# Kernel optimization log

Hardware: AMD Instinct MI355X
Metric: run time of the kernel (lower is better)

## Reference

```python
import jax, jax.numpy as jnp
import numpy as np

LAYERS = 30
LAYERS_PER_STACK = 10  # layers // stacks
UP_SCALES = (10, 8)


def setup_inputs() -> dict:
    key = jax.random.key(0)
    ks = jax.random.split(key, 12)
    B, T_c, C_in = 4, 400, 80
    T = T_c * UP_SCALES[0] * UP_SCALES[1]  # 32000
    OUT_CH, RES_CH, GATE_CH, SKIP_CH = 256, 64, 128, 64
    s = 0.05  # small init scale to keep gates unsaturated
    inp = {
        "x": jax.random.randint(ks[0], (B, T), 0, OUT_CH, dtype=jnp.int64),
        "c": jax.random.normal(ks[1], (B, C_in, T_c), dtype=jnp.float32),
        "first_w": jax.random.normal(ks[2], (RES_CH, OUT_CH), dtype=jnp.float32) * s,
        "first_b": jnp.zeros((RES_CH,), dtype=jnp.float32),
        "dconv_w": jax.random.normal(ks[3], (LAYERS, GATE_CH, RES_CH, 2), dtype=jnp.float32) * s,
        "dconv_b": jnp.zeros((LAYERS, GATE_CH), dtype=jnp.float32),
        "cond_w": jax.random.normal(ks[4], (LAYERS, GATE_CH, C_in), dtype=jnp.float32) * s,
        "skip_w": jax.random.normal(ks[5], (LAYERS, SKIP_CH, GATE_CH // 2), dtype=jnp.float32) * s,
        "skip_b": jnp.zeros((LAYERS, SKIP_CH), dtype=jnp.float32),
        "out_w": jax.random.normal(ks[6], (LAYERS, RES_CH, GATE_CH // 2), dtype=jnp.float32) * s,
        "out_b": jnp.zeros((LAYERS, RES_CH), dtype=jnp.float32),
        "last_w1": jax.random.normal(ks[7], (SKIP_CH, SKIP_CH), dtype=jnp.float32) * s,
        "last_b1": jnp.zeros((SKIP_CH,), dtype=jnp.float32),
        "last_w2": jax.random.normal(ks[8], (OUT_CH, SKIP_CH), dtype=jnp.float32) * s,
        "last_b2": jnp.zeros((OUT_CH,), dtype=jnp.float32),
        "conv_in_w": jax.random.normal(ks[9], (C_in, C_in), dtype=jnp.float32) * s,
        "up_w0": jnp.full((2 * UP_SCALES[0] + 1,), 1.0 / (2 * UP_SCALES[0] + 1), dtype=jnp.float32),
        "up_w1": jnp.full((2 * UP_SCALES[1] + 1,), 1.0 / (2 * UP_SCALES[1] + 1), dtype=jnp.float32),
    }
    return inp


def _upsample(c, conv_in_w, up_ws):
    # conv_in: 1x1 (aux_context_window=0)
    c = jnp.einsum('oc,bct->bot', conv_in_w, c)
    for w, scale in zip(up_ws, UP_SCALES):
        c = jnp.repeat(c, scale, axis=-1)  # nearest-neighbor upsample along time
        B, C, T = c.shape
        k = w.shape[0]
        c = jax.lax.conv_general_dilated(
            c.reshape(B * C, 1, T), w.reshape(1, 1, k),
            window_strides=(1,), padding=[(scale, scale)],
        ).reshape(B, C, T)
    return c


def reference(x, c, first_w, first_b, dconv_w, dconv_b, cond_w, skip_w, skip_b,
              out_w, out_b, last_w1, last_b1, last_w2, last_b2, conv_in_w, up_w0, up_w1):
    B, T = x.shape
    c_up = _upsample(c, conv_in_w, (up_w0, up_w1))  # (B, 80, T)
    # first_conv on one-hot(x): gather columns of first_w -> (B, 64, T)
    h = first_w.T[x].transpose(0, 2, 1) + first_b[None, :, None]
    skips = jnp.zeros_like(h[:, :1, :1])  # broadcastable accumulator
    skips = 0.0
    for l in range(LAYERS):
        d = 2 ** (l % LAYERS_PER_STACK)
        # causal dilated conv, kernel_size=2: y[t] = W0 @ h[t-d] + W1 @ h[t]
        h_prev = jnp.pad(h, ((0, 0), (0, 0), (d, 0)))[:, :, :T]
        y = (jnp.einsum('oc,bct->bot', dconv_w[l, :, :, 0], h_prev)
             + jnp.einsum('oc,bct->bot', dconv_w[l, :, :, 1], h)
             + dconv_b[l][None, :, None]
             + jnp.einsum('oc,bct->bot', cond_w[l], c_up))
        a, g = jnp.split(y, 2, axis=1)
        z = jnp.tanh(a) * jax.nn.sigmoid(g)  # gated activation, (B, 64, T)
        skips = skips + jnp.einsum('oc,bct->bot', skip_w[l], z) + skip_b[l][None, :, None]
        h = jnp.einsum('oc,bct->bot', out_w[l], z) + out_b[l][None, :, None] + h
    out = jax.nn.relu(skips)
    out = jnp.einsum('oc,bct->bot', last_w1, out) + last_b1[None, :, None]
    out = jax.nn.relu(out)
    out = jnp.einsum('oc,bct->bot', last_w2, out) + last_b2[None, :, None]
    return out  # (B, 256, T) logits
```

## Files before the change

### kernel.cpp

```cpp
#include <hip/hip_runtime.h>

#define TF 32000

typedef short s8v __attribute__((ext_vector_type(8)));
typedef float f4v __attribute__((ext_vector_type(4)));

__device__ __forceinline__ float us2f(unsigned int u16) {
  union { float f; unsigned int i; } v; v.i = u16 << 16; return v.f;
}
__device__ __forceinline__ unsigned short f2b(float f) {
  union { float f; unsigned int u; } v; v.f = f;
  unsigned int u = v.u;
  u = (u + 0x7fffu + ((u >> 16) & 1u)) >> 16;
  return (unsigned short)u;
}

__global__ void k_probe_x(const int* __restrict__ x, int* __restrict__ flag) {
  int acc = 0;
  for (int i = blockIdx.x * 256 + threadIdx.x; i < 64000; i += 32 * 256)
    acc |= x[2 * i + 1];
  unsigned long long m = __ballot(acc != 0);
  if ((threadIdx.x & 63) == 0 && m != 0ULL) atomicOr(flag, 1);
}

__global__ void k_probe_dt(const unsigned short* __restrict__ fw, int* __restrict__ flag) {
  int i = blockIdx.x * 256 + threadIdx.x;
  float v = us2f(fw[i]);
  int bad = !(fabsf(v) <= 1.0f);
  unsigned long long m = __ballot(bad);
  if ((threadIdx.x & 63) == 0 && m != 0ULL) atomicOr(flag, 2);
}

struct SrcPtrs { const void* p[17]; };

__global__ __launch_bounds__(256) void k_cvt(SrcPtrs sp, const int* __restrict__ flag,
                                             float* __restrict__ wdst, float* __restrict__ cdst) {
  int i = blockIdx.x * 256 + threadIdx.x;
  if (i >= 1223846) return;
  const bool f32 = ((*flag) & 2) != 0;
  int s, base;
  if (i < 507968) {
    if (i < 16384)       { s = 0;  base = 0; }
    else if (i < 16448)  { s = 1;  base = 16384; }
    else                 { s = 2;  base = 16448; }
  } else if (i < 943808) {
    if (i < 511808)      { s = 3;  base = 507968; }
    else if (i < 819008) { s = 4;  base = 511808; }
    else if (i < 941888) { s = 5;  base = 819008; }
    else                 { s = 6;  base = 941888; }
  } else if (i < 1089408) {
    if (i < 1066688)      { s = 7;  base = 943808; }
    else if (i < 1068608) { s = 8;  base = 1066688; }
    else if (i < 1072704) { s = 9;  base = 1068608; }
    else if (i < 1072768) { s = 10; base = 1072704; }
    else if (i < 1089152) { s = 11; base = 1072768; }
    else                  { s = 12; base = 1089152; }
  } else {
    if (i < 1095808)      { s = 13; base = 1089408; }
    else if (i < 1095829) { s = 14; base = 1095808; }
    else if (i < 1095846) { s = 15; base = 1095829; }
    else                  { s = 16; base = 1095846; }
  }
  int j = i - base;
  const void* src = sp.p[s];
  float v = f32 ? ((const float*)src)[j] : us2f(((const unsigned short*)src)[j]);
  if (s == 16) cdst[j] = v; else wdst[i] = v;
}

__global__ __launch_bounds__(256) void k_pack(const float* __restrict__ wc,
    unsigned short* __restrict__ w1h, unsigned short* __restrict__ w1l,
    unsigned short* __restrict__ w2h, unsigned short* __restrict__ w2l) {
  int i = blockIdx.x * 256 + threadIdx.x;
  if (i < 860160) {
    int l = i / 28672, r = i % 28672, o = r / 224, k = r % 224;
    float v = 0.f;
    if (k < 128)      v = wc[16448 + l * 16384 + o * 128 + (k & 63) * 2 + (k >> 6)];
    else if (k < 208) v = wc[511808 + l * 10240 + o * 80 + (k - 128)];
    unsigned short hh = f2b(v);
    w1h[i] = hh;
    w1l[i] = f2b(v - us2f(hh));
  } else if (i < 1105920) {
    int j = i - 860160;
    int l = j / 8192, r = j % 8192, o = r / 64, ch = r % 64;
    float v = (o < 64) ? wc[819008 + l * 4096 + o * 64 + ch]
                       : wc[943808 + l * 4096 + (o - 64) * 64 + ch];
    unsigned short hh = f2b(v);
    w2h[j] = hh;
    w2l[j] = f2b(v - us2f(hh));
  }
}

__global__ void k_convin(const float* __restrict__ c, const float* __restrict__ w,
                         float* __restrict__ c0) {
  int b = blockIdx.x / 400, t = blockIdx.x % 400;
  int o = threadIdx.x;
  if (o >= 80) return;
  const float* crow = c + b * 80 * 400 + t;
  const float* wrow = w + o * 80;
  float acc = 0.f;
  for (int k = 0; k < 80; ++k) acc += wrow[k] * crow[k * 400];
  c0[(b * 80 + o) * 400 + t] = acc;
}

__global__ void k_up1(const float* __restrict__ c0, const float* __restrict__ w,
                      float* __restrict__ s1) {
  int id = blockIdx.x * 256 + threadIdx.x;
  int t = id % 4000;
  int bc = id / 4000;
  const float* src = c0 + bc * 400;
  float acc = 0.f;
  #pragma unroll
  for (int j = 0; j < 21; ++j) {
    int tt = t - 10 + j;
    if (tt >= 0 && tt < 4000) acc += w[j] * src[tt / 10];
  }
  s1[id] = acc;
}

__global__ void k_up2(const float* __restrict__ s1, const float* __restrict__ w,
                      unsigned short* __restrict__ cup) {
  int id = blockIdx.x * 256 + threadIdx.x;
  int t = id % TF;
  int bc = id / TF;
  const float* src = s1 + bc * 4000;
  float acc = 0.f;
  #pragma unroll
  for (int j = 0; j < 17; ++j) {
    int tt = t - 8 + j;
    if (tt >= 0 && tt < TF) acc += w[j] * src[tt / 8];
  }
  cup[id] = f2b(acc);
}

__global__ void k_first(const int* __restrict__ x, const int* __restrict__ flag,
                        const float* __restrict__ fw, const float* __restrict__ fb,
                        float* __restrict__ h) {
  int id = blockIdx.x * 256 + threadIdx.x;
  int t = id % TF;
  int r = (id / TF) & 63;
  int b = id / (64 * TF);
  int i = b * TF + t;
  int idx = (((*flag) & 1) ? x[i] : x[2 * i]) & 255;
  h[id] = fw[r * 256 + idx] + fb[r];
}

__global__ __launch_bounds__(256, 3) void k_layer(
    const float* __restrict__ h_in, float* __restrict__ h_out,
    float* __restrict__ skips, const unsigned short* __restrict__ cup,
    const unsigned short* __restrict__ w1h, const unsigned short* __restrict__ w1l,
    const unsigned short* __restrict__ w2h, const unsigned short* __restrict__ w2l,
    const float* __restrict__ db, const float* __restrict__ sb,
    const float* __restrict__ ob, int d, int mode) {
  __shared__ __align__(16) unsigned char smem[47104];
  unsigned short (*Xhi)[232] = (unsigned short (*)[232])smem;
  unsigned short (*Xlo)[136] = (unsigned short (*)[136])(smem + 29696);
  unsigned short (*Zhi)[72]  = (unsigned short (*)[72])smem;
  unsigned short (*Zlo)[72]  = (unsigned short (*)[72])(smem + 9216);
  const int b = blockIdx.x / 500;
  const int t0 = (blockIdx.x % 500) * 64;
  const int tid = threadIdx.x;
  const float* hb = h_in + (size_t)b * 64 * TF;

  const bool d4 = (d & 3) == 0;
  for (int u = tid; u < 1024; u += 256) {
    const int arr = u >> 9, rem = u & 511, cp = rem >> 4, tq = rem & 15;
    const int ch0 = cp * 2;
    float va[4], vb[4];
    if (arr == 0) {
      float4 A = *(const float4*)(hb + ch0 * TF + t0 + tq * 4);
      float4 B = *(const float4*)(hb + (ch0 + 1) * TF + t0 + tq * 4);
      va[0] = A.x; va[1] = A.y; va[2] = A.z; va[3] = A.w;
      vb[0] = B.x; vb[1] = B.y; vb[2] = B.z; vb[3] = B.w;
    } else {
      const int base = t0 - d + tq * 4;
      if (d4 && base >= 0) {
        float4 A = *(const float4*)(hb + ch0 * TF + base);
        float4 B = *(const float4*)(hb + (ch0 + 1) * TF + base);
        va[0] = A.x; va[1] = A.y; va[2] = A.z; va[3] = A.w;
        vb[0] = B.x; vb[1] = B.y; vb[2] = B.z; vb[3] = B.w;
      } else {
        #pragma unroll
        for (int j = 0; j < 4; ++j) {
          int tp = base + j;
          va[j] = tp >= 0 ? hb[ch0 * TF + tp] : 0.f;
          vb[j] = tp >= 0 ? hb[(ch0 + 1) * TF + tp] : 0.f;
        }
      }
    }
    const int colb = (arr == 0 ? 64 : 0) + ch0;
    #pragma unroll
    for (int j = 0; j < 4; ++j) {
      int t = tq * 4 + j;
      unsigned int h0 = f2b(va[j]), h1 = f2b(vb[j]);
      float l0 = va[j] - us2f(h0), l1 = vb[j] - us2f(h1);
      *(unsigned int*)&Xhi[t][colb] = h0 | (h1 << 16);
      *(unsigned int*)&Xlo[t][colb] = (unsigned int)f2b(l0) | ((unsigned int)f2b(l1) << 16);
    }
  }
  const unsigned short* cb = cup + (size_t)b * 80 * TF;
  for (int u = tid; u < 640; u += 256) {
    const int cp = u >> 4, tq = u & 15, cc0 = cp * 2;
    const unsigned int* pa = (const unsigned int*)(cb + cc0 * TF + t0 + tq * 4);
    const unsigned int* pb = (const unsigned int*)(cb + (cc0 + 1) * TF + t0 + tq * 4);
    unsigned int a0 = pa[0], a1 = pa[1], b0 = pb[0], b1 = pb[1];
    const int colb = 128 + cc0, tb = tq * 4;
    *(unsigned int*)&Xhi[tb + 0][colb] = (a0 & 0xffffu) | (b0 << 16);
    *(unsigned int*)&Xhi[tb + 1][colb] = (a0 >> 16) | (b0 & 0xffff0000u);
    *(unsigned int*)&Xhi[tb + 2][colb] = (a1 & 0xffffu) | (b1 << 16);
    *(unsigned int*)&Xhi[tb + 3][colb] = (a1 >> 16) | (b1 & 0xffff0000u);
  }
  if (tid < 64) {
    s8v z = {0, 0, 0, 0, 0, 0, 0, 0};
    *(s8v*)&Xhi[tid][208] = z;
    *(s8v*)&Xhi[tid][216] = z;
  }
  __syncthreads();

  const int wv = tid >> 6, l15 = tid & 15, kl = (tid >> 4) & 3;
  const int R0 = wv * 16, R1 = 64 + wv * 16;
  const int ko = kl * 8;

  f4v accA[4], accG[4];
  {
    f4v bA = *(const f4v*)(db + R0 + kl * 4);
    f4v bG = *(const f4v*)(db + R1 + kl * 4);
    #pragma unroll
    for (int ct = 0; ct < 4; ++ct) { accA[ct] = bA; accG[ct] = bG; }
  }
  #pragma unroll
  for (int s = 0; s < 4; ++s) {
    const int k0 = s * 32 + ko;
    s8v ah0 = *(const s8v*)(w1h + (R0 + l15) * 224 + k0);
    s8v ah1 = *(const s8v*)(w1h + (R1 + l15) * 224 + k0);
    s8v al0 = *(const s8v*)(w1l + (R0 + l15) * 224 + k0);
    s8v al1 = *(const s8v*)(w1l + (R1 + l15) * 224 + k0);
    #pragma unroll
    for (int ct = 0; ct < 4; ++ct) {
      s8v bh = *(const s8v*)&Xhi[ct * 16 + l15][k0];
      s8v bl = *(const s8v*)&Xlo[ct * 16 + l15][k0];
      accA[ct] = __builtin_amdgcn_mfma_f32_16x16x32_bf16(ah0, bh, accA[ct], 0, 0, 0);
      accG[ct] = __builtin_amdgcn_mfma_f32_16x16x32_bf16(ah1, bh, accG[ct], 0, 0, 0);
      accA[ct] = __builtin_amdgcn_mfma_f32_16x16x32_bf16(al0, bh, accA[ct], 0, 0, 0);
      accG[ct] = __builtin_amdgcn_mfma_f32_16x16x32_bf16(al1, bh, accG[ct], 0, 0, 0);
      accA[ct] = __builtin_amdgcn_mfma_f32_16x16x32_bf16(ah0, bl, accA[ct], 0, 0, 0);
      accG[ct] = __builtin_amdgcn_mfma_f32_16x16x32_bf16(ah1, bl, accG[ct], 0, 0, 0);
    }
  }
  #pragma unroll
  for (int s = 4; s < 7; ++s) {
    const int k0 = s * 32 + ko;
    s8v ah0 = *(const s8v*)(w1h + (R0 + l15) * 224 + k0);
    s8v ah1 = *(const s8v*)(w1h + (R1 + l15) * 224 + k0);
    s8v al0 = *(const s8v*)(w1l + (R0 + l15) * 224 + k0);
    s8v al1 = *(const s8v*)(w1l + (R1 + l15) * 224 + k0);
    #pragma unroll
    for (int ct = 0; ct < 4; ++ct) {
      s8v bh = *(const s8v*)&Xhi[ct * 16 + l15][k0];
      accA[ct] = __builtin_amdgcn_mfma_f32_16x16x32_bf16(ah0, bh, accA[ct], 0, 0, 0);
      accG[ct] = __builtin_amdgcn_mfma_f32_16x16x32_bf16(ah1, bh, accG[ct], 0, 0, 0);
      accA[ct] = __builtin_amdgcn_mfma_f32_16x16x32_bf16(al0, bh, accA[ct], 0, 0, 0);
      accG[ct] = __builtin_amdgcn_mfma_f32_16x16x32_bf16(al1, bh, accG[ct], 0, 0, 0);
    }
  }

  float rres[16];
  #pragma unroll
  for (int ct = 0; ct < 4; ++ct) {
    const int t = ct * 16 + l15;
    uint2 rh = *(const uint2*)&Xhi[t][64 + R0 + kl * 4];
    uint2 rl = *(const uint2*)&Xlo[t][64 + R0 + kl * 4];
    rres[ct * 4 + 0] = us2f(rh.x & 0xffffu) + us2f(rl.x & 0xffffu);
    rres[ct * 4 + 1] = us2f(rh.x >> 16)     + us2f(rl.x >> 16);
    rres[ct * 4 + 2] = us2f(rh.y & 0xffffu) + us2f(rl.y & 0xffffu);
    rres[ct * 4 + 3] = us2f(rh.y >> 16)     + us2f(rl.y >> 16);
  }
  __syncthreads();

  #pragma unroll
  for (int ct = 0; ct < 4; ++ct) {
    const int t = ct * 16 + l15;
    unsigned int hw[2], lw[2];
    #pragma unroll
    for (int p = 0; p < 2; ++p) {
      float a0 = accA[ct][2 * p],     g0 = accG[ct][2 * p];
      float a1 = accA[ct][2 * p + 1], g1 = accG[ct][2 * p + 1];
      float z0 = tanhf(a0) / (1.f + expf(-g0));
      float z1 = tanhf(a1) / (1.f + expf(-g1));
      unsigned int h0 = f2b(z0), h1 = f2b(z1);
      hw[p] = h0 | (h1 << 16);
      lw[p] = (unsigned int)f2b(z0 - us2f(h0)) | ((unsigned int)f2b(z1 - us2f(h1)) << 16);
    }
    uint2 hv; hv.x = hw[0]; hv.y = hw[1];
    uint2 lv; lv.x = lw[0]; lv.y = lw[1];
    *(uint2*)&Zhi[t][R0 + kl * 4] = hv;
    *(uint2*)&Zlo[t][R0 + kl * 4] = lv;
  }
  __syncthreads();

  f4v accS[4], accH[4];
  {
    f4v bS = *(const f4v*)(sb + R0 + kl * 4);
    f4v bO = *(const f4v*)(ob + R0 + kl * 4);
    #pragma unroll
    for (int ct = 0; ct < 4; ++ct) { accS[ct] = bS; accH[ct] = bO; }
  }
  #pragma unroll
  for (int s = 0; s < 2; ++s) {
    const int k0 = s * 32 + ko;
    s8v ah0 = *(const s8v*)(w2h + (R0 + l15) * 64 + k0);
    s8v ah1 = *(const s8v*)(w2h + (R1 + l15) * 64 + k0);
    s8v al0 = *(const s8v*)(w2l + (R0 + l15) * 64 + k0);
    s8v al1 = *(const s8v*)(w2l + (R1 + l15) * 64 + k0);
    #pragma unroll
    for (int ct = 0; ct < 4; ++ct) {
      s8v bh = *(const s8v*)&Zhi[ct * 16 + l15][k0];
      s8v bl = *(const s8v*)&Zlo[ct * 16 + l15][k0];
      accS[ct] = __builtin_amdgcn_mfma_f32_16x16x32_bf16(ah0, bh, accS[ct], 0, 0, 0);
      accH[ct] = __builtin_amdgcn_mfma_f32_16x16x32_bf16(ah1, bh, accH[ct], 0, 0, 0);
      accS[ct] = __builtin_amdgcn_mfma_f32_16x16x32_bf16(al0, bh, accS[ct], 0, 0, 0);
      accH[ct] = __builtin_amdgcn_mfma_f32_16x16x32_bf16(al1, bh, accH[ct], 0, 0, 0);
      accS[ct] = __builtin_amdgcn_mfma_f32_16x16x32_bf16(ah0, bl, accS[ct], 0, 0, 0);
      accH[ct] = __builtin_amdgcn_mfma_f32_16x16x32_bf16(ah1, bl, accH[ct], 0, 0, 0);
    }
  }

  float* sp_ = skips + ((size_t)b * 64 + R0 + kl * 4) * TF + t0;
  float* hp_ = h_out + ((size_t)b * 64 + R0 + kl * 4) * TF + t0;
  #pragma unroll
  for (int ct = 0; ct < 4; ++ct) {
    const int t = ct * 16 + l15;
    if (mode & 1) {
      sp_[0 * TF + t] = accS[ct][0];
      sp_[1 * TF + t] = accS[ct][1];
      sp_[2 * TF + t] = accS[ct][2];
      sp_[3 * TF + t] = accS[ct][3];
    } else {
      sp_[0 * TF + t] += accS[ct][0];
      sp_[1 * TF + t] += accS[ct][1];
      sp_[2 * TF + t] += accS[ct][2];
      sp_[3 * TF + t] += accS[ct][3];
    }
    if (!(mode & 2)) {
      hp_[0 * TF + t] = accH[ct][0] + rres[ct * 4 + 0];
      hp_[1 * TF + t] = accH[ct][1] + rres[ct * 4 + 1];
      hp_[2 * TF + t] = accH[ct][2] + rres[ct * 4 + 2];
      hp_[3 * TF + t] = accH[ct][3] + rres[ct * 4 + 3];
    }
  }
}

__global__ __launch_bounds__(256, 4) void k_final(
    const float* __restrict__ skips,
    const float* __restrict__ w1, const float* __restrict__ b1,
    const float* __restrict__ w2, const float* __restrict__ b2,
    float* __restrict__ out) {
  __shared__ __align__(16) unsigned short Shi[64][72];
  __shared__ __align__(16) unsigned short Slo[64][72];
  __shared__ __align__(16) unsigned short Zhi[64][72];
  __shared__ __align__(16) unsigned short Zlo[64][72];
  const int b = blockIdx.x / 500;
  const int t0 = (blockIdx.x % 500) * 64;
  const int tid = threadIdx.x;
  const float* sbase = skips + (size_t)b * 64 * TF;

  for (int u = tid; u < 512; u += 256) {
    const int cp = u >> 4, tq = u & 15, ch0 = cp * 2;
    float4 A = *(const float4*)(sbase + (size_t)ch0 * TF + t0 + tq * 4);
    float4 B = *(const float4*)(sbase + (size_t)(ch0 + 1) * TF + t0 + tq * 4);
    float va[4] = {fmaxf(A.x, 0.f), fmaxf(A.y, 0.f), fmaxf(A.z, 0.f), fmaxf(A.w, 0.f)};
    float vb[4] = {fmaxf(B.x, 0.f), fmaxf(B.y, 0.f), fmaxf(B.z, 0.f), fmaxf(B.w, 0.f)};
    #pragma unroll
    for (int j = 0; j < 4; ++j) {
      int t = tq * 4 + j;
      unsigned int h0 = f2b(va[j]), h1 = f2b(vb[j]);
      *(unsigned int*)&Shi[t][ch0] = h0 | (h1 << 16);
      *(unsigned int*)&Slo[t][ch0] =
          (unsigned int)f2b(va[j] - us2f(h0)) | ((unsigned int)f2b(vb[j] - us2f(h1)) << 16);
    }
  }
  __syncthreads();

  const int wv = tid >> 6, l15 = tid & 15, kl = (tid >> 4) & 3;
  const int R = wv * 16;

  f4v acc[4];
  {
    f4v bb = *(const f4v*)(b1 + R + kl * 4);
    #pragma unroll
    for (int ct = 0; ct < 4; ++ct) acc[ct] = bb;
  }
  #pragma unroll
  for (int ks = 0; ks < 2; ++ks) {
    const int k0 = ks * 32 + kl * 8;
    const float* wr = w1 + (R + l15) * 64 + k0;
    s8v ah, al;
    #pragma unroll
    for (int m = 0; m < 8; ++m) {
      float v = wr[m];
      unsigned short hh = f2b(v);
      ah[m] = (short)hh;
      al[m] = (short)f2b(v - us2f(hh));
    }
    #pragma unroll
    for (int ct = 0; ct < 4; ++ct) {
      s8v bh = *(const s8v*)&Shi[ct * 16 + l15][k0];
      s8v bl = *(const s8v*)&Slo[ct * 16 + l15][k0];
      acc[ct] = __builtin_amdgcn_mfma_f32_16x16x32_bf16(ah, bh, acc[ct], 0, 0, 0);
      acc[ct] = __builtin_amdgcn_mfma_f32_16x16x32_bf16(al, bh, acc[ct], 0, 0, 0);
      acc[ct] = __builtin_amdgcn_mfma_f32_16x16x32_bf16(ah, bl, acc[ct], 0, 0, 0);
    }
  }
  #pragma unroll
  for (int ct = 0; ct < 4; ++ct) {
    const int t = ct * 16 + l15;
    unsigned int hw[2], lw[2];
    #pragma unroll
    for (int p = 0; p < 2; ++p) {
      float z0 = fmaxf(acc[ct][2 * p], 0.f);
      float z1 = fmaxf(acc[ct][2 * p + 1], 0.f);
      unsigned int h0 = f2b(z0), h1 = f2b(z1);
      hw[p] = h0 | (h1 << 16);
      lw[p] = (unsigned int)f2b(z0 - us2f(h0)) | ((unsigned int)f2b(z1 - us2f(h1)) << 16);
    }
    uint2 hv; hv.x = hw[0]; hv.y = hw[1];
    uint2 lv; lv.x = lw[0]; lv.y = lw[1];
    *(uint2*)&Zhi[t][R + kl * 4] = hv;
    *(uint2*)&Zlo[t][R + kl * 4] = lv;
  }
  __syncthreads();

  float* obase = out + (size_t)b * 256 * TF + t0;
  #pragma unroll
  for (int g = 0; g < 4; ++g) {
    const int R2 = g * 64 + wv * 16;
    f4v a2[4];
    {
      f4v bb = *(const f4v*)(b2 + R2 + kl * 4);
      #pragma unroll
      for (int ct = 0; ct < 4; ++ct) a2[ct] = bb;
    }
    #pragma unroll
    for (int ks = 0; ks < 2; ++ks) {
      const int k0 = ks * 32 + kl * 8;
      const float* wr = w2 + (R2 + l15) * 64 + k0;
      s8v ah, al;
      #pragma unroll
      for (int m = 0; m < 8; ++m) {
        float v = wr[m];
        unsigned short hh = f2b(v);
        ah[m] = (short)hh;
        al[m] = (short)f2b(v - us2f(hh));
      }
      #pragma unroll
      for (int ct = 0; ct < 4; ++ct) {
        s8v bh = *(const s8v*)&Zhi[ct * 16 + l15][k0];
        s8v bl = *(const s8v*)&Zlo[ct * 16 + l15][k0];
        a2[ct] = __builtin_amdgcn_mfma_f32_16x16x32_bf16(ah, bh, a2[ct], 0, 0, 0);
        a2[ct] = __builtin_amdgcn_mfma_f32_16x16x32_bf16(al, bh, a2[ct], 0, 0, 0);
        a2[ct] = __builtin_amdgcn_mfma_f32_16x16x32_bf16(ah, bl, a2[ct], 0, 0, 0);
      }
    }
    const int r0 = R2 + kl * 4;
    #pragma unroll
    for (int ct = 0; ct < 4; ++ct) {
      const int t = ct * 16 + l15;
      obase[(size_t)(r0 + 0) * TF + t] = a2[ct][0];
      obase[(size_t)(r0 + 1) * TF + t] = a2[ct][1];
      obase[(size_t)(r0 + 2) * TF + t] = a2[ct][2];
      obase[(size_t)(r0 + 3) * TF + t] = a2[ct][3];
    }
  }
}

extern "C" void kernel_launch(void* const* d_in, const int* in_sizes, int n_in,
                              void* d_out, int out_size, void* d_ws, size_t ws_size,
                              hipStream_t stream) {
  const int* x = (const int*)d_in[0];

  float* ws = (float*)d_ws;
  int*   flag = (int*)ws;
  float* wcan = ws + 16;
  unsigned short* cupb = (unsigned short*)(ws + 1095872);
  float* ha    = ws + 6215872;
  float* hbuf  = ws + 14407872;
  float* skips = ws + 22599872;
  float* cin = ha;
  float* c0  = ha + 128000;
  float* s1f = ha + 256000;
  if (ws_size < (size_t)30791872 * 4) return;

  float* fwc = wcan;            float* fbc = wcan + 16384;
  float* dbc = wcan + 507968;
  float* sbc = wcan + 941888;
  float* obc = wcan + 1066688;  float* w1c = wcan + 1068608;
  float* b1c = wcan + 1072704;  float* w2c = wcan + 1072768;
  float* b2c = wcan + 1089152;  float* ciwc = wcan + 1089408;
  float* uw0c = wcan + 1095808; float* uw1c = wcan + 1095829;

  unsigned short* wp = (unsigned short*)d_out;
  unsigned short* W1H = wp;
  unsigned short* W1L = wp + 860160;
  unsigned short* W2H = wp + 1720320;
  unsigned short* W2L = wp + 1966080;

  hipMemsetAsync(flag, 0, 64, stream);
  k_probe_x<<<dim3(32), dim3(256), 0, stream>>>(x, flag);
  k_probe_dt<<<dim3(64), dim3(256), 0, stream>>>((const unsigned short*)d_in[2], flag);

  SrcPtrs sp;
  sp.p[0] = d_in[2];  sp.p[1] = d_in[3];  sp.p[2] = d_in[4];  sp.p[3] = d_in[5];
  sp.p[4] = d_in[6];  sp.p[5] = d_in[7];  sp.p[6] = d_in[8];  sp.p[7] = d_in[9];
  sp.p[8] = d_in[10]; sp.p[9] = d_in[11]; sp.p[10] = d_in[12]; sp.p[11] = d_in[13];
  sp.p[12] = d_in[14]; sp.p[13] = d_in[15]; sp.p[14] = d_in[16]; sp.p[15] = d_in[17];
  sp.p[16] = d_in[1];
  k_cvt<<<dim3(4781), dim3(256), 0, stream>>>(sp, flag, wcan, cin);
  k_pack<<<dim3(4320), dim3(256), 0, stream>>>(wcan, W1H, W1L, W2H, W2L);

  k_convin<<<dim3(1600), dim3(128), 0, stream>>>(cin, ciwc, c0);
  k_up1<<<dim3(5000), dim3(256), 0, stream>>>(c0, uw0c, s1f);
  k_up2<<<dim3(40000), dim3(256), 0, stream>>>(s1f, uw1c, cupb);
  k_first<<<dim3(32000), dim3(256), 0, stream>>>(x, flag, fwc, fbc, ha);

  float* hin = ha; float* hout = hbuf;
  for (int l = 0; l < 30; ++l) {
    int d = 1 << (l % 10);
    int mode = (l == 0 ? 1 : 0) | (l == 29 ? 2 : 0);
    k_layer<<<dim3(2000), dim3(256), 0, stream>>>(
        hin, hout, skips, cupb,
        W1H + (size_t)l * 28672, W1L + (size_t)l * 28672,
        W2H + (size_t)l * 8192,  W2L + (size_t)l * 8192,
        dbc + l * 128, sbc + l * 64, obc + l * 64, d, mode);
    float* t = hin; hin = hout; hout = t;
  }
  k_final<<<dim3(2000), dim3(256), 0, stream>>>(skips, w1c, b1c, w2c, b2c,
                                                (float*)d_out);
}
```

Measured before the change: 1.938 ms.

## Store residual state as pre-split channel-paired bf16 hi/lo and use fast gate math

The residual stream h is now kept between layers as channel-pair-packed bf16 hi/lo words instead of fp32. Each layer loads those words with 16-byte vector loads straight into shared memory, and the hi/lo split moves to the producer's epilogue. The conditioning tensor is packed by channel pairs in the same way. Load index mapping is reorganised for coalescing, and tanh*sigmoid is replaced with a clamped exp/rcp formulation. The goal is less per-layer conversion ALU work and simpler loads, at the cost of slightly different gate accuracy.

```diff
diff --git a/kernel.cpp b/kernel.cpp
--- a/kernel.cpp
+++ b/kernel.cpp
@@ -4,6 +4,7 @@
 
 typedef short s8v __attribute__((ext_vector_type(8)));
 typedef float f4v __attribute__((ext_vector_type(4)));
+typedef unsigned int ui4 __attribute__((ext_vector_type(4)));
 
 __device__ __forceinline__ float us2f(unsigned int u16) {
   union { float f; unsigned int i; } v; v.i = u16 << 16; return v.f;
@@ -13,6 +14,12 @@
   unsigned int u = v.u;
   u = (u + 0x7fffu + ((u >> 16) & 1u)) >> 16;
   return (unsigned short)u;
+}
+__device__ __forceinline__ float gatef(float a, float g) {
+  a = fminf(fmaxf(a, -15.f), 15.f);
+  float ta = __expf(2.f * a);
+  float sg = __expf(-g);
+  return (ta - 1.f) * __builtin_amdgcn_rcpf((ta + 1.f) * (1.f + sg));
 }
 
 __global__ void k_probe_x(const int* __restrict__ x, int* __restrict__ flag) {
@@ -118,35 +125,47 @@
 }
 
 __global__ void k_up2(const float* __restrict__ s1, const float* __restrict__ w,
-                      unsigned short* __restrict__ cup) {
+                      unsigned int* __restrict__ cpk) {
   int id = blockIdx.x * 256 + threadIdx.x;
   int t = id % TF;
-  int bc = id / TF;
-  const float* src = s1 + bc * 4000;
-  float acc = 0.f;
+  int cp = (id / TF) % 40;
+  int b = id / (40 * TF);
+  const float* src0 = s1 + (b * 80 + cp * 2) * 4000;
+  const float* src1 = src0 + 4000;
+  float a0 = 0.f, a1 = 0.f;
   #pragma unroll
   for (int j = 0; j < 17; ++j) {
     int tt = t - 8 + j;
-    if (tt >= 0 && tt < TF) acc += w[j] * src[tt / 8];
-  }
-  cup[id] = f2b(acc);
+    if (tt >= 0 && tt < TF) {
+      int q = tt / 8;
+      a0 += w[j] * src0[q];
+      a1 += w[j] * src1[q];
+    }
+  }
+  cpk[id] = (unsigned int)f2b(a0) | ((unsigned int)f2b(a1) << 16);
 }
 
 __global__ void k_first(const int* __restrict__ x, const int* __restrict__ flag,
                         const float* __restrict__ fw, const float* __restrict__ fb,
-                        float* __restrict__ h) {
+                        unsigned int* __restrict__ hhi, unsigned int* __restrict__ hlo) {
   int id = blockIdx.x * 256 + threadIdx.x;
   int t = id % TF;
-  int r = (id / TF) & 63;
-  int b = id / (64 * TF);
+  int rp = (id / TF) & 31;
+  int b = id / (32 * TF);
   int i = b * TF + t;
   int idx = (((*flag) & 1) ? x[i] : x[2 * i]) & 255;
-  h[id] = fw[r * 256 + idx] + fb[r];
+  int r0 = rp * 2;
+  float v0 = fw[r0 * 256 + idx] + fb[r0];
+  float v1 = fw[(r0 + 1) * 256 + idx] + fb[r0 + 1];
+  unsigned int h0 = f2b(v0), h1 = f2b(v1);
+  hhi[id] = h0 | (h1 << 16);
+  hlo[id] = (unsigned int)f2b(v0 - us2f(h0)) | ((unsigned int)f2b(v1 - us2f(h1)) << 16);
 }
 
 __global__ __launch_bounds__(256, 3) void k_layer(
-    const float* __restrict__ h_in, float* __restrict__ h_out,
-    float* __restrict__ skips, const unsigned short* __restrict__ cup,
+    const unsigned int* __restrict__ hhi_in, const unsigned int* __restrict__ hlo_in,
+    unsigned int* __restrict__ hhi_out, unsigned int* __restrict__ hlo_out,
+    float* __restrict__ skips, const unsigned int* __restrict__ cpk,
     const unsigned short* __restrict__ w1h, const unsigned short* __restrict__ w1l,
     const unsigned short* __restrict__ w2h, const unsigned short* __restrict__ w2l,
     const float* __restrict__ db, const float* __restrict__ sb,
@@ -159,55 +178,52 @@
   const int b = blockIdx.x / 500;
   const int t0 = (blockIdx.x % 500) * 64;
   const int tid = threadIdx.x;
-  const float* hb = h_in + (size_t)b * 64 * TF;
+  const unsigned int* hhiB = hhi_in + (size_t)b * 32 * TF;
+  const unsigned int* hloB = hlo_in + (size_t)b * 32 * TF;
 
   const bool d4 = (d & 3) == 0;
   for (int u = tid; u < 1024; u += 256) {
-    const int arr = u >> 9, rem = u & 511, cp = rem >> 4, tq = rem & 15;
-    const int ch0 = cp * 2;
-    float va[4], vb[4];
+    const int g = u & 63, blk = u >> 6;
+    const int cp = (g & 7) | ((blk & 3) << 3);
+    const int tq = (g >> 3) | ((blk & 4) << 1);
+    const int arr = blk >> 3;
+    const int row = cp * TF;
+    ui4 hv, lv;
     if (arr == 0) {
-      float4 A = *(const float4*)(hb + ch0 * TF + t0 + tq * 4);
-      float4 B = *(const float4*)(hb + (ch0 + 1) * TF + t0 + tq * 4);
-      va[0] = A.x; va[1] = A.y; va[2] = A.z; va[3] = A.w;
-      vb[0] = B.x; vb[1] = B.y; vb[2] = B.z; vb[3] = B.w;
+      hv = *(const ui4*)(hhiB + row + t0 + tq * 4);
+      lv = *(const ui4*)(hloB + row + t0 + tq * 4);
     } else {
       const int base = t0 - d + tq * 4;
       if (d4 && base >= 0) {
-        float4 A = *(const float4*)(hb + ch0 * TF + base);
-        float4 B = *(const float4*)(hb + (ch0 + 1) * TF + base);
-        va[0] = A.x; va[1] = A.y; va[2] = A.z; va[3] = A.w;
-        vb[0] = B.x; vb[1] = B.y; vb[2] = B.z; vb[3] = B.w;
+        hv = *(const ui4*)(hhiB + row + base);
+        lv = *(const ui4*)(hloB + row + base);
       } else {
         #pragma unroll
         for (int j = 0; j < 4; ++j) {
           int tp = base + j;
-          va[j] = tp >= 0 ? hb[ch0 * TF + tp] : 0.f;
-          vb[j] = tp >= 0 ? hb[(ch0 + 1) * TF + tp] : 0.f;
+          hv[j] = tp >= 0 ? hhiB[row + tp] : 0u;
+          lv[j] = tp >= 0 ? hloB[row + tp] : 0u;
         }
       }
     }
-    const int colb = (arr == 0 ? 64 : 0) + ch0;
+    const int colb = (arr ? 0 : 64) + cp * 2;
     #pragma unroll
     for (int j = 0; j < 4; ++j) {
-      int t = tq * 4 + j;
-      unsigned int h0 = f2b(va[j]), h1 = f2b(vb[j]);
-      float l0 = va[j] - us2f(h0), l1 = vb[j] - us2f(h1);
-      *(unsigned int*)&Xhi[t][colb] = h0 | (h1 << 16);
-      *(unsigned int*)&Xlo[t][colb] = (unsigned int)f2b(l0) | ((unsigned int)f2b(l1) << 16);
-    }
-  }
-  const unsigned short* cb = cup + (size_t)b * 80 * TF;
+      const int t = tq * 4 + j;
+      *(unsigned int*)&Xhi[t][colb] = hv[j];
+      *(unsigned int*)&Xlo[t][colb] = lv[j];
+    }
+  }
+  const unsigned int* cpkB = cpk + (size_t)b * 40 * TF;
   for (int u = tid; u < 640; u += 256) {
-    const int cp = u >> 4, tq = u & 15, cc0 = cp * 2;
-    const unsigned int* pa = (const unsigned int*)(cb + cc0 * TF + t0 + tq * 4);
-    const unsigned int* pb = (const unsigned int*)(cb + (cc0 + 1) * TF + t0 + tq * 4);
-    unsigned int a0 = pa[0], a1 = pa[1], b0 = pb[0], b1 = pb[1];
-    const int colb = 128 + cc0, tb = tq * 4;
-    *(unsigned int*)&Xhi[tb + 0][colb] = (a0 & 0xffffu) | (b0 << 16);
-    *(unsigned int*)&Xhi[tb + 1][colb] = (a0 >> 16) | (b0 & 0xffff0000u);
-    *(unsigned int*)&Xhi[tb + 2][colb] = (a1 & 0xffffu) | (b1 << 16);
-    *(unsigned int*)&Xhi[tb + 3][colb] = (a1 >> 16) | (b1 & 0xffff0000u);
+    const int g = u & 63, blk = u >> 6;
+    const int cp = (g & 7) | ((blk % 5) << 3);
+    const int tq = (g >> 3) | ((blk / 5) << 3);
+    ui4 cv = *(const ui4*)(cpkB + cp * TF + t0 + tq * 4);
+    const int colb = 128 + cp * 2;
+    #pragma unroll
+    for (int j = 0; j < 4; ++j)
+      *(unsigned int*)&Xhi[tq * 4 + j][colb] = cv[j];
   }
   if (tid < 64) {
     s8v z = {0, 0, 0, 0, 0, 0, 0, 0};
@@ -282,10 +298,8 @@
     unsigned int hw[2], lw[2];
     #pragma unroll
     for (int p = 0; p < 2; ++p) {
-      float a0 = accA[ct][2 * p],     g0 = accG[ct][2 * p];
-      float a1 = accA[ct][2 * p + 1], g1 = accG[ct][2 * p + 1];
-      float z0 = tanhf(a0) / (1.f + expf(-g0));
-      float z1 = tanhf(a1) / (1.f + expf(-g1));
+      float z0 = gatef(accA[ct][2 * p],     accG[ct][2 * p]);
+      float z1 = gatef(accA[ct][2 * p + 1], accG[ct][2 * p + 1]);
       unsigned int h0 = f2b(z0), h1 = f2b(z1);
       hw[p] = h0 | (h1 << 16);
       lw[p] = (unsigned int)f2b(z0 - us2f(h0)) | ((unsigned int)f2b(z1 - us2f(h1)) << 16);
@@ -324,8 +338,10 @@
     }
   }
 
-  float* sp_ = skips + ((size_t)b * 64 + R0 + kl * 4) * TF + t0;
-  float* hp_ = h_out + ((size_t)b * 64 + R0 + kl * 4) * TF + t0;
+  const int r0 = R0 + kl * 4, p0 = r0 >> 1;
+  float* sp_ = skips + ((size_t)b * 64 + r0) * TF + t0;
+  unsigned int* hho = hhi_out + ((size_t)b * 32 + p0) * TF + t0;
+  unsigned int* hlo = hlo_out + ((size_t)b * 32 + p0) * TF + t0;
   #pragma unroll
   for (int ct = 0; ct < 4; ++ct) {
     const int t = ct * 16 + l15;
@@ -341,10 +357,15 @@
       sp_[3 * TF + t] += accS[ct][3];
     }
     if (!(mode & 2)) {
-      hp_[0 * TF + t] = accH[ct][0] + rres[ct * 4 + 0];
-      hp_[1 * TF + t] = accH[ct][1] + rres[ct * 4 + 1];
-      hp_[2 * TF + t] = accH[ct][2] + rres[ct * 4 + 2];
-      hp_[3 * TF + t] = accH[ct][3] + rres[ct * 4 + 3];
+      float h0 = accH[ct][0] + rres[ct * 4 + 0];
+      float h1 = accH[ct][1] + rres[ct * 4 + 1];
+      float h2 = accH[ct][2] + rres[ct * 4 + 2];
+      float h3 = accH[ct][3] + rres[ct * 4 + 3];
+      unsigned int a0 = f2b(h0), a1 = f2b(h1), a2 = f2b(h2), a3 = f2b(h3);
+      hho[t]      = a0 | (a1 << 16);
+      hho[TF + t] = a2 | (a3 << 16);
+      hlo[t]      = (unsigned int)f2b(h0 - us2f(a0)) | ((unsigned int)f2b(h1 - us2f(a1)) << 16);
+      hlo[TF + t] = (unsigned int)f2b(h2 - us2f(a2)) | ((unsigned int)f2b(h3 - us2f(a3)) << 16);
     }
   }
 }
@@ -480,7 +501,7 @@
   float* ws = (float*)d_ws;
   int*   flag = (int*)ws;
   float* wcan = ws + 16;
-  unsigned short* cupb = (unsigned short*)(ws + 1095872);
+  unsigned int* cpkb = (unsigned int*)(ws + 1095872);
   float* ha    = ws + 6215872;
   float* hbuf  = ws + 14407872;
   float* skips = ws + 22599872;
@@ -488,6 +509,11 @@
   float* c0  = ha + 128000;
   float* s1f = ha + 256000;
   if (ws_size < (size_t)30791872 * 4) return;
+
+  unsigned int* haHi = (unsigned int*)ha;
+  unsigned int* haLo = haHi + 4096000;
+  unsigned int* hbHi = (unsigned int*)hbuf;
+  unsigned int* hbLo = hbHi + 4096000;
 
   float* fwc = wcan;            float* fbc = wcan + 16384;
   float* dbc = wcan + 507968;
@@ -518,19 +544,22 @@
 
   k_convin<<<dim3(1600), dim3(128), 0, stream>>>(cin, ciwc, c0);
   k_up1<<<dim3(5000), dim3(256), 0, stream>>>(c0, uw0c, s1f);
-  k_up2<<<dim3(40000), dim3(256), 0, stream>>>(s1f, uw1c, cupb);
-  k_first<<<dim3(32000), dim3(256), 0, stream>>>(x, flag, fwc, fbc, ha);
-
-  float* hin = ha; float* hout = hbuf;
+  k_up2<<<dim3(20000), dim3(256), 0, stream>>>(s1f, uw1c, cpkb);
+  k_first<<<dim3(16000), dim3(256), 0, stream>>>(x, flag, fwc, fbc, haHi, haLo);
+
+  unsigned int* hiIn = haHi; unsigned int* loIn = haLo;
+  unsigned int* hiOut = hbHi; unsigned int* loOut = hbLo;
   for (int l = 0; l < 30; ++l) {
     int d = 1 << (l % 10);
     int mode = (l == 0 ? 1 : 0) | (l == 29 ? 2 : 0);
     k_layer<<<dim3(2000), dim3(256), 0, stream>>>(
-        hin, hout, skips, cupb,
+        hiIn, loIn, hiOut, loOut, skips, cpkb,
         W1H + (size_t)l * 28672, W1L + (size_t)l * 28672,
         W2H + (size_t)l * 8192,  W2L + (size_t)l * 8192,
         dbc + l * 128, sbc + l * 64, obc + l * 64, d, mode);
-    float* t = hin; hin = hout; hout = t;
+    unsigned int* t;
+    t = hiIn; hiIn = hiOut; hiOut = t;
+    t = loIn; loIn = loOut; loOut = t;
   }
   k_final<<<dim3(2000), dim3(256), 0, stream>>>(skips, w1c, b1c, w2c, b2c,
                                                 (float*)d_out);
```

After: 1.906 ms. Within noise of the previous version (-1.7%).
